# Performance work log

Hardware: AMD Instinct MI355X
Metric: run time of the kernel (lower is better)

Reference implementation:

```python
import jax, jax.numpy as jnp
import numpy as np

N_NODES = 50000
N_EDGES = 800000
DIM = 128


def setup_inputs() -> dict:
    key = jax.random.key(0)
    k_x, k_e, k_w1, k_w2 = jax.random.split(key, 4)
    x = jax.random.normal(k_x, (N_NODES, DIM), dtype=jnp.float32)
    edge_index = jax.random.randint(k_e, (2, N_EDGES), 0, N_NODES, dtype=jnp.int64)
    scale = 1.0 / np.sqrt(DIM)
    W1 = jax.random.normal(k_w1, (DIM, DIM), dtype=jnp.float32) * scale
    b1 = jnp.zeros((DIM,), dtype=jnp.float32)
    W2 = jax.random.normal(k_w2, (DIM, DIM), dtype=jnp.float32) * scale
    b2 = jnp.zeros((DIM,), dtype=jnp.float32)
    return {"x": x, "edge_index": edge_index, "W1": W1, "b1": b1, "W2": W2, "b2": b2}


def _gcn_conv(x, W, b, src, dst, n_nodes):
    """PyG GCNConv: D^{-1/2}(A+I)D^{-1/2} (x @ W) + b, self-loops added."""
    h = x @ W  # [N, D]
    ones = jnp.ones(src.shape[0], dtype=h.dtype)
    # degree of A+I, counting incoming edges at target nodes plus self-loop
    deg = jax.ops.segment_sum(ones, dst, num_segments=n_nodes) + 1.0
    dinv = jax.lax.rsqrt(deg)  # [N]
    norm = dinv[src] * dinv[dst]  # [E]
    msgs = h[src] * norm[:, None]  # [E, D] gather (memory-bound)
    agg = jax.ops.segment_sum(msgs, dst, num_segments=n_nodes)  # scatter-add
    agg = agg + h * (dinv * dinv)[:, None]  # self-loop contribution
    return agg + b


def reference(x, edge_index, W1, b1, W2, b2):
    src, dst = edge_index[0], edge_index[1]
    n = x.shape[0]
    identity = x
    out = jax.nn.relu(_gcn_conv(x, W1, b1, src, dst, n))
    out = _gcn_conv(out, W2, b2, src, dst, n)
    return jax.nn.relu(out + identity)
```

## Files before the change

### kernel.cpp

```cpp
#include <hip/hip_runtime.h>

#define N_NODES 50000
#define N_EDGES 800000
#define DIM 128
#define NB 391
#define CAP 2560
#define BIN_CHUNK 4096
#define BIN_BLOCKS 196

typedef unsigned int uint;
typedef unsigned short ushort;
typedef __attribute__((ext_vector_type(8))) __bf16 bf16x8;
typedef __attribute__((ext_vector_type(4))) float f32x4;

__device__ __forceinline__ uint f2bf(float f) {
    uint u = __float_as_uint(f);
    return (u + 0x7FFFu + ((u >> 16) & 1u)) >> 16;
}
__device__ __forceinline__ float2 bf2f2(uint u) {
    return make_float2(__uint_as_float(u << 16), __uint_as_float(u & 0xFFFF0000u));
}


__global__ __launch_bounds__(256) void prep_kernel(const float* __restrict__ W1,
                                                   const float* __restrict__ W2,
                                                   uint* __restrict__ Wt1,
                                                   uint* __restrict__ Wt2,
                                                   int* __restrict__ bincursor) {
    int idx = blockIdx.x * 256 + threadIdx.x;
    if (idx < 16384) {
        const float* W = (idx < 8192) ? W1 : W2;
        uint* Wt = (idx < 8192) ? Wt1 : Wt2;
        int i = idx & 8191;
        int n = i >> 6, k2 = i & 63;
        uint lo = f2bf(W[(2 * k2) * DIM + n]);
        uint hi = f2bf(W[(2 * k2 + 1) * DIM + n]);
        Wt[i] = lo | (hi << 16);
    } else {
        int b = idx - 16384;
        if (b < NB) bincursor[b] = b * CAP;
    }
}


__global__ __launch_bounds__(256) void bin_kernel(const int* __restrict__ ei,
                                                  int* __restrict__ bincursor,
                                                  uint* __restrict__ pairs) {
    __shared__ int lh[NB];
    __shared__ int lbase[NB];
    int t = threadIdx.x;
    int eb = blockIdx.x * BIN_CHUNK;

    for (int b = t; b < NB; b += 256) lh[b] = 0;
    __syncthreads();

    int s_reg[16], d_reg[16];
#pragma unroll
    for (int i = 0; i < 16; ++i) {
        int e = eb + i * 256 + t;
        if (e < N_EDGES) {
            s_reg[i] = ei[e];
            d_reg[i] = ei[N_EDGES + e];
            atomicAdd(&lh[d_reg[i] >> 7], 1);
        } else {
            d_reg[i] = -1;
        }
    }
    __syncthreads();

    for (int b = t; b < NB; b += 256) {
        int c = lh[b];
        lbase[b] = c ? atomicAdd(&bincursor[b], c) : 0;
    }
    __syncthreads();
    for (int b = t; b < NB; b += 256) lh[b] = 0;
    __syncthreads();

#pragma unroll
    for (int i = 0; i < 16; ++i) {
        int d = d_reg[i];
        if (d >= 0) {
            int bin = d >> 7;
            int r = atomicAdd(&lh[bin], 1);
            pairs[lbase[bin] + r] = ((uint)s_reg[i] << 7) | (uint)(d & 127);
        }
    }
}


__global__ __launch_bounds__(256) void fill2_kernel(const uint* __restrict__ pairs,
                                                    const int* __restrict__ bincursor,
                                                    int* __restrict__ rowbeg,
                                                    int* __restrict__ rowend,
                                                    float* __restrict__ dinv,
                                                    int* __restrict__ csr_src) {
    __shared__ int deg[128];
    __shared__ int sc[128];
    __shared__ int cur[128];
    int t = threadIdx.x;
    int blk = blockIdx.x;
    int bs = blk * CAP;
    int be = bincursor[blk];

    if (t < 128) deg[t] = 0;
    __syncthreads();

    for (int p = bs + t; p < be; p += 256) atomicAdd(&deg[pairs[p] & 127u], 1);
    __syncthreads();

    if (t < 128) sc[t] = deg[t];
    __syncthreads();
#pragma unroll
    for (int off = 1; off < 128; off <<= 1) {
        int v = (t < 128 && t >= off) ? sc[t - off] : 0;
        __syncthreads();
        if (t < 128) sc[t] += v;
        __syncthreads();
    }

    if (t < 128) {
        int ex = sc[t] - deg[t];
        cur[t] = ex;
        int node = blk * 128 + t;
        if (node < N_NODES) {
            rowbeg[node] = bs + ex;
            rowend[node] = bs + sc[t];
            dinv[node] = rsqrtf((float)deg[t] + 1.0f);
        }
    }
    __syncthreads();

    for (int p = bs + t; p < be; p += 256) {
        uint sd = pairs[p];
        int r = atomicAdd(&cur[sd & 127u], 1);
        csr_src[bs + r] = (int)(sd >> 7);
    }
}


template <bool ABF>
__global__ __launch_bounds__(256) void mgemm_kernel(const void* __restrict__ Xv,
                                                    const uint* __restrict__ Wt,
                                                    const float* __restrict__ dinv,
                                                    uint* __restrict__ Hs) {
    int t = threadIdx.x;
    int wv = t >> 6;
    int l = t & 63;
    int col = l & 15;
    int g = l >> 4;
    int r0 = blockIdx.x * 64 + wv * 16;

    int ar = r0 + col;
    if (ar > N_NODES - 1) ar = N_NODES - 1;

    bf16x8 a[4];
    if (ABF) {
        const uint4* Xr = (const uint4*)((const uint*)Xv + (size_t)ar * 64);
#pragma unroll
        for (int kk = 0; kk < 4; ++kk) a[kk] = __builtin_bit_cast(bf16x8, Xr[kk * 4 + g]);
    } else {
        const float4* Xr = (const float4*)((const float*)Xv + (size_t)ar * DIM);
#pragma unroll
        for (int kk = 0; kk < 4; ++kk) {
            float4 x0 = Xr[kk * 8 + g * 2];
            float4 x1 = Xr[kk * 8 + g * 2 + 1];
            uint4 p;
            p.x = f2bf(x0.x) | (f2bf(x0.y) << 16);
            p.y = f2bf(x0.z) | (f2bf(x0.w) << 16);
            p.z = f2bf(x1.x) | (f2bf(x1.y) << 16);
            p.w = f2bf(x1.z) | (f2bf(x1.w) << 16);
            a[kk] = __builtin_bit_cast(bf16x8, p);
        }
    }

    const uint4* Wr = (const uint4*)Wt;
    f32x4 acc[8];
#pragma unroll
    for (int n = 0; n < 8; ++n) acc[n] = (f32x4){0.f, 0.f, 0.f, 0.f};

#pragma unroll
    for (int n = 0; n < 8; ++n) {
        const uint4* wrow = Wr + (size_t)(n * 16 + col) * 16;
#pragma unroll
        for (int kk = 0; kk < 4; ++kk) {
            bf16x8 b = __builtin_bit_cast(bf16x8, wrow[kk * 4 + g]);
            acc[n] = __builtin_amdgcn_mfma_f32_16x16x32_bf16(a[kk], b, acc[n], 0, 0, 0);
        }
    }

#pragma unroll
    for (int j = 0; j < 4; ++j) {
        int row = r0 + g * 4 + j;
        if (row < N_NODES) {
            float di = dinv[row];
            ushort* hrow = (ushort*)(Hs + (size_t)row * 64);
#pragma unroll
            for (int n = 0; n < 8; ++n) {
                hrow[n * 16 + col] = (ushort)f2bf(acc[n][j] * di);
            }
        }
    }
}


template <bool RES, bool OBF>
__global__ __launch_bounds__(256) void agg_kernel(const int* __restrict__ rowbeg,
                                                  const int* __restrict__ rowend,
                                                  const int* __restrict__ csr_src,
                                                  const uint* __restrict__ Hs,
                                                  const float* __restrict__ dinv,
                                                  const float* __restrict__ b,
                                                  const float* __restrict__ resid,
                                                  void* __restrict__ outv) {
    int wave = (int)((blockIdx.x * (size_t)blockDim.x + threadIdx.x) >> 6);
    int lane = threadIdx.x & 63;
    int grp = lane >> 4;
    int li = lane & 15;
    int node = wave * 4 + grp;

    int beg = rowbeg[node];
    int end = rowend[node];

    const uint4* H4 = (const uint4*)Hs;
    float a0, a1, a2, a3, a4, a5, a6, a7;
    {
        uint4 su = H4[(size_t)node * 16 + li];
        float2 v0 = bf2f2(su.x), v1 = bf2f2(su.y), v2 = bf2f2(su.z), v3 = bf2f2(su.w);
        a0 = v0.x; a1 = v0.y; a2 = v1.x; a3 = v1.y;
        a4 = v2.x; a5 = v2.y; a6 = v3.x; a7 = v3.y;
    }

#define ADD8(u)                                                                   \
    {                                                                             \
        float2 v0 = bf2f2(u.x), v1 = bf2f2(u.y), v2 = bf2f2(u.z), v3 = bf2f2(u.w);\
        a0 += v0.x; a1 += v0.y; a2 += v1.x; a3 += v1.y;                           \
        a4 += v2.x; a5 += v2.y; a6 += v3.x; a7 += v3.y;                           \
    }

    int e = beg;
    for (; e + 1 < end; e += 2) {
        int s0 = csr_src[e];
        int s1 = csr_src[e + 1];
        uint4 u0 = H4[(size_t)s0 * 16 + li];
        uint4 u1 = H4[(size_t)s1 * 16 + li];
        ADD8(u0);
        ADD8(u1);
    }
    if (e < end) {
        int s = csr_src[e];
        uint4 u = H4[(size_t)s * 16 + li];
        ADD8(u);
    }
#undef ADD8

    float di = dinv[node];
    const float4* B4 = (const float4*)b;
    float4 bb0 = B4[li * 2], bb1 = B4[li * 2 + 1];
    float r0 = a0 * di + bb0.x, r1 = a1 * di + bb0.y;
    float r2 = a2 * di + bb0.z, r3 = a3 * di + bb0.w;
    float r4 = a4 * di + bb1.x, r5 = a5 * di + bb1.y;
    float r6 = a6 * di + bb1.z, r7 = a7 * di + bb1.w;

    if (OBF) {
        uint4 o;
        o.x = f2bf(fmaxf(r0, 0.f)) | (f2bf(fmaxf(r1, 0.f)) << 16);
        o.y = f2bf(fmaxf(r2, 0.f)) | (f2bf(fmaxf(r3, 0.f)) << 16);
        o.z = f2bf(fmaxf(r4, 0.f)) | (f2bf(fmaxf(r5, 0.f)) << 16);
        o.w = f2bf(fmaxf(r6, 0.f)) | (f2bf(fmaxf(r7, 0.f)) << 16);
        ((uint4*)outv)[(size_t)node * 16 + li] = o;
    } else {
        if (RES) {
            const float4* R4 = (const float4*)(resid + (size_t)node * DIM);
            float4 x0 = R4[li * 2], x1 = R4[li * 2 + 1];
            r0 += x0.x; r1 += x0.y; r2 += x0.z; r3 += x0.w;
            r4 += x1.x; r5 += x1.y; r6 += x1.z; r7 += x1.w;
        }
        float4* O4 = (float4*)((float*)outv + (size_t)node * DIM);
        O4[li * 2] = make_float4(fmaxf(r0, 0.f), fmaxf(r1, 0.f), fmaxf(r2, 0.f), fmaxf(r3, 0.f));
        O4[li * 2 + 1] = make_float4(fmaxf(r4, 0.f), fmaxf(r5, 0.f), fmaxf(r6, 0.f), fmaxf(r7, 0.f));
    }
}


extern "C" void kernel_launch(void* const* d_in, const int* in_sizes, int n_in,
                              void* d_out, int out_size, void* d_ws, size_t ws_size,
                              hipStream_t stream) {
    const float* x = (const float*)d_in[0];
    const int* edge_index = (const int*)d_in[1];
    const float* W1 = (const float*)d_in[2];
    const float* b1 = (const float*)d_in[3];
    const float* W2 = (const float*)d_in[4];
    const float* b2 = (const float*)d_in[5];
    float* out = (float*)d_out;

    char* ws = (char*)d_ws;
    int*   bincursor = (int*)(ws + 0);
    float* dinv      = (float*)(ws + (64 << 10));
    int*   rowbeg    = (int*)(ws + (320 << 10));
    int*   rowend    = (int*)(ws + (576 << 10));
    int*   csr_src   = (int*)(ws + (1 << 20));
    uint*  pairs     = (uint*)(ws + (6 << 20));
    uint*  Hs        = (uint*)(ws + (11 << 20));
    uint*  out1b     = (uint*)(ws + (24 << 20));
    uint*  Wt1       = (uint*)(ws + (37 << 20));
    uint*  Wt2       = (uint*)(ws + (37 << 20) + (64 << 10));

    prep_kernel<<<66, 256, 0, stream>>>(W1, W2, Wt1, Wt2, bincursor);
    bin_kernel<<<BIN_BLOCKS, 256, 0, stream>>>(edge_index, bincursor, pairs);
    fill2_kernel<<<NB, 256, 0, stream>>>(pairs, bincursor, rowbeg, rowend, dinv, csr_src);

    const int gemm_grid = (N_NODES + 63) / 64;
    const int agg_grid = (N_NODES / 4 + 3) / 4;

    mgemm_kernel<false><<<gemm_grid, 256, 0, stream>>>(x, Wt1, dinv, Hs);
    agg_kernel<false, true><<<agg_grid, 256, 0, stream>>>(rowbeg, rowend, csr_src, Hs, dinv, b1,
                                                          nullptr, out1b);

    mgemm_kernel<true><<<gemm_grid, 256, 0, stream>>>(out1b, Wt2, dinv, Hs);
    agg_kernel<true, false><<<agg_grid, 256, 0, stream>>>(rowbeg, rowend, csr_src, Hs, dinv, b2,
                                                          x, out);
}
```

Baseline: 146.4 us.

## Sort CSR neighbours by source chunk and unroll aggregation gather by four

The CSR fill now counts edges per (destination, source-range chunk) and scatters them so that each node's neighbour list is grouped by source-index chunk (pr>>20 splits sources into 7 ranges). Neighbouring aggregation rows then touch similar regions of H at the same time, which is meant to improve L2 locality for the gathers. The aggregation loop is also unrolled to four gathers per iteration to keep more loads in flight. The agg grid expression is replaced with the literal it already evaluated to. The costs are extra shared memory and a larger per-node prefix walk in fill2.

Measured after the change: 139.3 us. 1.05x faster.

```diff
diff --git a/kernel.cpp b/kernel.cpp
--- a/kernel.cpp
+++ b/kernel.cpp
@@ -5,6 +5,7 @@
 #define DIM 128
 #define NB 391
 #define CAP 2560
+#define NCH 7
 #define BIN_CHUNK 4096
 #define BIN_BLOCKS 196
 
@@ -94,46 +95,61 @@
                                                     int* __restrict__ rowend,
                                                     float* __restrict__ dinv,
                                                     int* __restrict__ csr_src) {
-    __shared__ int deg[128];
-    __shared__ int sc[128];
-    __shared__ int cur[128];
+    __shared__ int cnt[128 * 8];
+    __shared__ int nsum[128];
+    __shared__ int nbase[128];
     int t = threadIdx.x;
     int blk = blockIdx.x;
     int bs = blk * CAP;
     int be = bincursor[blk];
 
-    if (t < 128) deg[t] = 0;
-    __syncthreads();
-
-    for (int p = bs + t; p < be; p += 256) atomicAdd(&deg[pairs[p] & 127u], 1);
-    __syncthreads();
-
-    if (t < 128) sc[t] = deg[t];
+    for (int i = t; i < 128 * 8; i += 256) cnt[i] = 0;
+    __syncthreads();
+
+    for (int p = bs + t; p < be; p += 256) {
+        uint pr = pairs[p];
+        atomicAdd(&cnt[(pr & 127u) * 8 + (pr >> 20)], 1);
+    }
+    __syncthreads();
+
+    if (t < 128) {
+        int s = 0;
+#pragma unroll
+        for (int c = 0; c < NCH; ++c) s += cnt[t * 8 + c];
+        nsum[t] = s;
+        nbase[t] = s;
+    }
     __syncthreads();
 #pragma unroll
     for (int off = 1; off < 128; off <<= 1) {
-        int v = (t < 128 && t >= off) ? sc[t - off] : 0;
+        int v = (t < 128 && t >= off) ? nbase[t - off] : 0;
         __syncthreads();
-        if (t < 128) sc[t] += v;
+        if (t < 128) nbase[t] += v;
         __syncthreads();
     }
 
     if (t < 128) {
-        int ex = sc[t] - deg[t];
-        cur[t] = ex;
+        int ex = nbase[t] - nsum[t];
         int node = blk * 128 + t;
         if (node < N_NODES) {
             rowbeg[node] = bs + ex;
-            rowend[node] = bs + sc[t];
-            dinv[node] = rsqrtf((float)deg[t] + 1.0f);
+            rowend[node] = bs + nbase[t];
+            dinv[node] = rsqrtf((float)nsum[t] + 1.0f);
+        }
+        int run = ex;
+#pragma unroll
+        for (int c = 0; c < NCH; ++c) {
+            int v = cnt[t * 8 + c];
+            cnt[t * 8 + c] = run;
+            run += v;
         }
     }
     __syncthreads();
 
     for (int p = bs + t; p < be; p += 256) {
-        uint sd = pairs[p];
-        int r = atomicAdd(&cur[sd & 127u], 1);
-        csr_src[bs + r] = (int)(sd >> 7);
+        uint pr = pairs[p];
+        int r = atomicAdd(&cnt[(pr & 127u) * 8 + (pr >> 20)], 1);
+        csr_src[bs + r] = (int)(pr >> 7);
     }
 }
 
@@ -238,15 +254,18 @@
     }
 
     int e = beg;
-    for (; e + 1 < end; e += 2) {
-        int s0 = csr_src[e];
-        int s1 = csr_src[e + 1];
+    for (; e + 3 < end; e += 4) {
+        int s0 = csr_src[e], s1 = csr_src[e + 1], s2 = csr_src[e + 2], s3 = csr_src[e + 3];
         uint4 u0 = H4[(size_t)s0 * 16 + li];
         uint4 u1 = H4[(size_t)s1 * 16 + li];
+        uint4 u2 = H4[(size_t)s2 * 16 + li];
+        uint4 u3 = H4[(size_t)s3 * 16 + li];
         ADD8(u0);
         ADD8(u1);
-    }
-    if (e < end) {
+        ADD8(u2);
+        ADD8(u3);
+    }
+    for (; e < end; ++e) {
         int s = csr_src[e];
         uint4 u = H4[(size_t)s * 16 + li];
         ADD8(u);
@@ -310,7 +329,7 @@
     fill2_kernel<<<NB, 256, 0, stream>>>(pairs, bincursor, rowbeg, rowend, dinv, csr_src);
 
     const int gemm_grid = (N_NODES + 63) / 64;
-    const int agg_grid = (N_NODES / 4 + 3) / 4;
+    const int agg_grid = 3125;
 
     mgemm_kernel<false><<<gemm_grid, 256, 0, stream>>>(x, Wt1, dinv, Hs);
     agg_kernel<false, true><<<agg_grid, 256, 0, stream>>>(rowbeg, rowend, csr_src, Hs, dinv, b1,
```
